# Kernel tuning notes

Hardware: AMD Instinct MI355X
Metric: run time of the kernel (lower is better)

The kernel has to match this reference:

```python
import jax, jax.numpy as jnp
import numpy as np

VOCAB = 32000
EMB_DIM = 64
BATCH, SEQ = 2, 4096


def setup_inputs() -> dict:
    key = jax.random.key(0)
    kx, kw = jax.random.split(key)
    x = jax.random.normal(kx, (BATCH, SEQ, EMB_DIM), dtype=jnp.float32)
    W = jax.random.normal(kw, (VOCAB, EMB_DIM), dtype=jnp.float32)
    return {"x": x, "W": W}


def reference(x, W):
    # x: [B, S, D] continuous embeddings; W: [V, D] embedding table.
    B, S, D = x.shape
    A = x.reshape(-1, D)                       # [N, D], N = B*S
    # cosine similarity: (A @ W^T) / (|A| |W|)
    nom = A @ W.T                              # [N, V]  (huge intermediate)
    norm_A = jnp.linalg.norm(A, axis=1)        # [N]
    norm_W = jnp.linalg.norm(W, axis=1)        # [V]
    sims = nom / (norm_A[:, None] * norm_W[None, :])
    idx = jnp.argmax(sims, axis=-1)            # [N]
    idx = idx.reshape(B, S)
    onehot = jax.nn.one_hot(idx, W.shape[0], dtype=jnp.float32)  # [B, S, V]
    return onehot
```

## Files before the change

kernel.cpp:

```cpp
#include <hip/hip_runtime.h>

#define VOCAB 32000
#define EMB 64
#define NROWS 8192
#define NSUB 500
#define SUBPAD 512
#define PAT 57
#define K2_BLOCKS 3648
#define NZ2 2048
#define K1_SETUP 125
#define K1_ZERO 875
#define K1_ITERS 28
#define K1_F4 (K1_ZERO * 256 * K1_ITERS)
#define TOTAL_F4 (NROWS * (VOCAB / 4))
#define K2_F4 (TOTAL_F4 - K1_F4)

typedef __attribute__((ext_vector_type(8))) short bf16x8;
typedef __attribute__((ext_vector_type(4))) float f32x4;
typedef float f4nt __attribute__((ext_vector_type(4)));

__device__ __forceinline__ unsigned enc_f32(float f) {
    unsigned u = __float_as_uint(f);
    return (u & 0x80000000u) ? ~u : (u | 0x80000000u);
}
__device__ __forceinline__ float dec_f32(unsigned e) {
    unsigned u = (e & 0x80000000u) ? (e & 0x7fffffffu) : ~e;
    return __uint_as_float(u);
}
__device__ __forceinline__ unsigned short f2bf(float f) {
    unsigned u = __float_as_uint(f);
    return (unsigned short)((u + 0x7fffu + ((u >> 16) & 1u)) >> 16);
}

__global__ __launch_bounds__(256) void k1_kernel(
    const float* __restrict__ x, const float* __restrict__ W,
    unsigned short* __restrict__ A16, unsigned short* __restrict__ WB16,
    float* __restrict__ invn, float* __restrict__ normA,
    float4* __restrict__ out4)
{
    const int bx = blockIdx.x;
    if (bx >= K1_SETUP) {
        const int zid = bx - K1_SETUP;
        const f4nt z = {0.f, 0.f, 0.f, 0.f};
        float4* p = out4 + (size_t)zid * 256 + threadIdx.x;
        #pragma unroll 4
        for (int j = 0; j < K1_ITERS; ++j)
            __builtin_nontemporal_store(z, (f4nt*)(p + (size_t)j * (K1_ZERO * 256)));
        return;
    }
    int i = bx * 256 + threadIdx.x;
    if (i < VOCAB) {
        const float4* w4 = (const float4*)(W + (size_t)i * EMB);
        float4 buf[16];
        float s = 0.f;
        #pragma unroll
        for (int q = 0; q < 16; ++q) {
            float4 w = w4[q]; buf[q] = w;
            s += w.x * w.x + w.y * w.y + w.z * w.z + w.w * w.w;
        }
        float inv = 1.0f / sqrtf(s);
        invn[i] = inv;
        ushort4* dst = (ushort4*)(WB16 + (size_t)i * EMB);
        #pragma unroll
        for (int q = 0; q < 16; ++q) {
            float4 w = buf[q];
            ushort4 u;
            u.x = f2bf(w.x * inv); u.y = f2bf(w.y * inv);
            u.z = f2bf(w.z * inv); u.w = f2bf(w.w * inv);
            dst[q] = u;
        }
    }
    if (i < NROWS) {
        const float4* a4 = (const float4*)(x + (size_t)i * EMB);
        float4 buf[16];
        float s = 0.f;
        #pragma unroll
        for (int q = 0; q < 16; ++q) {
            float4 a = a4[q]; buf[q] = a;
            s += a.x * a.x + a.y * a.y + a.z * a.z + a.w * a.w;
        }
        normA[i] = sqrtf(s);
        ushort4* dst = (ushort4*)(A16 + (size_t)i * EMB);
        #pragma unroll
        for (int q = 0; q < 16; ++q) {
            float4 a = buf[q];
            ushort4 u;
            u.x = f2bf(a.x); u.y = f2bf(a.y); u.z = f2bf(a.z); u.w = f2bf(a.w);
            dst[q] = u;
        }
    }
}

#define LOAD_GROUP(buf, base)                                            \
    {                                                                    \
        _Pragma("unroll")                                                \
        for (int tt = 0; tt < 4; ++tt) {                                 \
            buf[tt][0] = *(const bf16x8*)((base) + tt * 16 * EMB);       \
            buf[tt][1] = *(const bf16x8*)((base) + tt * 16 * EMB + 32);  \
        }                                                                \
    }
#define COMPUTE_GROUP(buf)                                               \
    {                                                                    \
        _Pragma("unroll")                                                \
        for (int tt = 0; tt < 4; ++tt) {                                 \
            _Pragma("unroll")                                            \
            for (int r = 0; r < 4; ++r) {                                \
                f32x4 acc = {0.f, 0.f, 0.f, 0.f};                        \
                acc = __builtin_amdgcn_mfma_f32_16x16x32_bf16(           \
                    a[r][0], buf[tt][0], acc, 0, 0, 0);                  \
                acc = __builtin_amdgcn_mfma_f32_16x16x32_bf16(           \
                    a[r][1], buf[tt][1], acc, 0, 0, 0);                  \
                _Pragma("unroll")                                        \
                for (int j = 0; j < 4; ++j)                              \
                    best[r][j] = fmaxf(best[r][j], acc[j]);              \
            }                                                            \
        }                                                                \
    }
#define STORE_SUB(sub)                                                   \
    {                                                                    \
        _Pragma("unroll")                                                \
        for (int r = 0; r < 4; ++r) {                                    \
            _Pragma("unroll")                                            \
            for (int j = 0; j < 4; ++j) {                                \
                float v = best[r][j];                                    \
                v = fmaxf(v, __shfl_xor(v, 1));                          \
                v = fmaxf(v, __shfl_xor(v, 2));                          \
                v = fmaxf(v, __shfl_xor(v, 4));                          \
                v = fmaxf(v, __shfl_xor(v, 8));                          \
                if (lr == 0)                                             \
                    pval[(size_t)(m0 + r * 16 + lg * 4 + j) * SUBPAD +   \
                         (sub)] = (unsigned short)(enc_f32(v) >> 16);    \
                best[r][j] = -3e38f;                                     \
            }                                                            \
        }                                                                \
    }

__global__ __launch_bounds__(256) void k2_kernel(
    const unsigned short* __restrict__ A16,
    const unsigned short* __restrict__ WB16,
    unsigned short* __restrict__ pval, float4* __restrict__ out4)
{
    const int bx = blockIdx.x;
    const int pat = bx / PAT, off = bx - pat * PAT;

    if (off >= 25) {
        const int zid = pat * 32 + (off - 25);
        const f4nt z = {0.f, 0.f, 0.f, 0.f};
        float4* base = out4 + K1_F4;
        unsigned i = (unsigned)zid * 256u + threadIdx.x;
        const unsigned stride = (unsigned)NZ2 * 256u;
        for (; i < (unsigned)K2_F4; i += stride)
            __builtin_nontemporal_store(z, (f4nt*)(base + i));
        return;
    }

    const int cid = pat * 25 + off;
    const int rowblk = cid & 31, chunk = cid >> 5;
    const int lane = threadIdx.x & 63, wid = threadIdx.x >> 6;
    const int lr = lane & 15, lg = lane >> 4;
    const int m0 = rowblk * 256 + wid * 64;
    const int n0 = chunk * 640;

    bf16x8 a[4][2];
    #pragma unroll
    for (int r = 0; r < 4; ++r)
        #pragma unroll
        for (int kk = 0; kk < 2; ++kk)
            a[r][kk] = *(const bf16x8*)(A16 + (size_t)(m0 + r * 16 + lr) * EMB + kk * 32 + lg * 8);

    float best[4][4];
    #pragma unroll
    for (int r = 0; r < 4; ++r)
        #pragma unroll
        for (int j = 0; j < 4; ++j) best[r][j] = -3e38f;

    const unsigned short* wb = WB16 + (size_t)(n0 + lr) * EMB + lg * 8;
    bf16x8 cb[4][2], nb[4][2];
    LOAD_GROUP(cb, wb);
    #pragma unroll
    for (int gp = 0; gp < 5; ++gp) {
        LOAD_GROUP(nb, wb + 64 * EMB);
        COMPUTE_GROUP(cb);
        STORE_SUB(chunk * 10 + gp * 2);
        wb += 64 * EMB;
        LOAD_GROUP(cb, wb + 64 * EMB);
        COMPUTE_GROUP(nb);
        STORE_SUB(chunk * 10 + gp * 2 + 1);
        wb += 64 * EMB;
    }
}

__global__ __launch_bounds__(64) void finalize_kernel(
    const float* __restrict__ x, const float* __restrict__ W,
    const float* __restrict__ invn, const unsigned short* __restrict__ pval,
    const float* __restrict__ normA, float* __restrict__ out)
{
    const int row = blockIdx.x;
    const int lane = threadIdx.x;
    __shared__ float xs[EMB];
    xs[lane] = x[(size_t)row * EMB + lane];

    const unsigned short* pr = pval + (size_t)row * SUBPAD + lane * 8;
    ushort4 v0 = *(const ushort4*)(pr);
    ushort4 v1 = *(const ushort4*)(pr + 4);
    unsigned short vals[8] = {v0.x, v0.y, v0.z, v0.w, v1.x, v1.y, v1.z, v1.w};

    unsigned mx = 0;
    #pragma unroll
    for (int k = 0; k < 8; ++k)
        if (lane * 8 + k < NSUB) mx = mx > (unsigned)vals[k] ? mx : (unsigned)vals[k];
    #pragma unroll
    for (int off = 1; off < 64; off <<= 1) {
        unsigned o = __shfl_xor(mx, off);
        mx = mx > o ? mx : o;
    }
    float thr = dec_f32(mx << 16) - 0.009f * normA[row];
    unsigned thr_enc = enc_f32(thr);

    __syncthreads();
    const float4* xs4 = (const float4*)xs;
    unsigned long long best = 0ull;

    #pragma unroll
    for (int k = 0; k < 8; ++k) {
        int sub = lane * 8 + k;
        bool c = (sub < NSUB) && ((((unsigned)vals[k] + 1u) << 16) > thr_enc);
        unsigned long long m = __ballot(c);
        while (m) {
            int src = __ffsll((long long)m) - 1;
            m &= m - 1;
            unsigned v = ((unsigned)(src * 8 + k)) * 64u + (unsigned)lane;
            const float4* w4 = (const float4*)(W + (size_t)v * EMB);
            float p0 = 0.f, p1 = 0.f, p2 = 0.f, p3 = 0.f;
            #pragma unroll
            for (int q = 0; q < 16; ++q) {
                float4 aa = xs4[q]; float4 ww = w4[q];
                p0 = fmaf(aa.x, ww.x, p0);
                p1 = fmaf(aa.y, ww.y, p1);
                p2 = fmaf(aa.z, ww.z, p2);
                p3 = fmaf(aa.w, ww.w, p3);
            }
            float s = ((p0 + p1) + (p2 + p3)) * invn[v];
            unsigned long long kk =
                ((unsigned long long)enc_f32(s) << 32) | (unsigned)(~v);
            best = best > kk ? best : kk;
        }
    }
    #pragma unroll
    for (int off = 1; off < 64; off <<= 1) {
        unsigned long long o = __shfl_xor(best, off);
        best = best > o ? best : o;
    }
    if (lane == 0)
        out[(size_t)row * VOCAB + (size_t)(unsigned)(~(unsigned)best)] = 1.0f;
}

extern "C" void kernel_launch(void* const* d_in, const int* in_sizes, int n_in,
                              void* d_out, int out_size, void* d_ws, size_t ws_size,
                              hipStream_t stream) {
    const float* x = (const float*)d_in[0];
    const float* W = (const float*)d_in[1];
    float* out = (float*)d_out;

    char* ws = (char*)d_ws;
    unsigned short* WB16 = (unsigned short*)(ws);
    unsigned short* A16  = (unsigned short*)(ws + 4096000);
    float* invn          = (float*)(ws + 5144576);
    float* normA         = (float*)(ws + 5272576);
    unsigned short* pval = (unsigned short*)(ws + 5305344);

    k1_kernel<<<dim3(K1_SETUP + K1_ZERO), dim3(256), 0, stream>>>(
        x, W, A16, WB16, invn, normA, (float4*)out);

    k2_kernel<<<dim3(K2_BLOCKS), dim3(256), 0, stream>>>(
        A16, WB16, pval, (float4*)out);

    finalize_kernel<<<dim3(NROWS), dim3(64), 0, stream>>>(
        x, W, invn, pval, normA, out);
}
```

Before: 252.5 us.

## Overlap output zeroing with finalize stage and defer one-hot writes to new kernel

Shifts part of the output zero-fill out of k1 and k2 into the finalize kernel, which now interleaves zeroing blocks with 4-row-per-block argmax refinement blocks. The winning index per row goes to a workspace buffer, and a tiny fourth kernel writes the one-hot 1.0 values after all zeroing is done. The goal is to hide memory-bound zero stores behind the latency-bound refinement work and to widen finalize blocks. The cost is an extra launch and a hardcoded K2_F4 that must agree with k2's zeroing range.

New measurement: 244.6 us. 1.03x faster.

```diff
diff --git a/kernel.cpp b/kernel.cpp
--- a/kernel.cpp
+++ b/kernel.cpp
@@ -5,15 +5,19 @@
 #define NROWS 8192
 #define NSUB 500
 #define SUBPAD 512
+#define K1_SETUP 125
+#define K1_ZERO 875
+#define K1_ITERS 21
+#define K1_F4 (K1_ZERO * 256 * K1_ITERS)
 #define PAT 57
 #define K2_BLOCKS 3648
 #define NZ2 2048
-#define K1_SETUP 125
-#define K1_ZERO 875
-#define K1_ITERS 28
-#define K1_F4 (K1_ZERO * 256 * K1_ITERS)
+#define K2_F4 51360000
+#define K3_BLOCKS 3072
+#define NZ3 1024
+#define K3_BASE (K1_F4 + K2_F4)
+#define K3_F4 9472000
 #define TOTAL_F4 (NROWS * (VOCAB / 4))
-#define K2_F4 (TOTAL_F4 - K1_F4)
 
 typedef __attribute__((ext_vector_type(8))) short bf16x8;
 typedef __attribute__((ext_vector_type(4))) float f32x4;
@@ -43,7 +47,7 @@
         const int zid = bx - K1_SETUP;
         const f4nt z = {0.f, 0.f, 0.f, 0.f};
         float4* p = out4 + (size_t)zid * 256 + threadIdx.x;
-        #pragma unroll 4
+        #pragma unroll 3
         for (int j = 0; j < K1_ITERS; ++j)
             __builtin_nontemporal_store(z, (f4nt*)(p + (size_t)j * (K1_ZERO * 256)));
         return;
@@ -190,15 +194,32 @@
     }
 }
 
-__global__ __launch_bounds__(64) void finalize_kernel(
+__global__ __launch_bounds__(256) void k3_kernel(
     const float* __restrict__ x, const float* __restrict__ W,
     const float* __restrict__ invn, const unsigned short* __restrict__ pval,
-    const float* __restrict__ normA, float* __restrict__ out)
+    const float* __restrict__ normA, unsigned long long* __restrict__ fin,
+    float4* __restrict__ out4)
 {
-    const int row = blockIdx.x;
-    const int lane = threadIdx.x;
-    __shared__ float xs[EMB];
-    xs[lane] = x[(size_t)row * EMB + lane];
+    const int bx = blockIdx.x;
+    const int pat = bx / 3, off = bx - pat * 3;
+
+    if (off == 2) {
+        const int zid = pat;
+        const f4nt z = {0.f, 0.f, 0.f, 0.f};
+        float4* base = out4 + K3_BASE;
+        unsigned i = (unsigned)zid * 256u + threadIdx.x;
+        const unsigned stride = (unsigned)NZ3 * 256u;
+        for (; i < (unsigned)K3_F4; i += stride)
+            __builtin_nontemporal_store(z, (f4nt*)(base + i));
+        return;
+    }
+
+    const int fid = pat * 2 + off;
+    const int wid = threadIdx.x >> 6, lane = threadIdx.x & 63;
+    const int row = fid * 4 + wid;
+
+    __shared__ float xs[4][EMB];
+    xs[wid][lane] = x[(size_t)row * EMB + lane];
 
     const unsigned short* pr = pval + (size_t)row * SUBPAD + lane * 8;
     ushort4 v0 = *(const ushort4*)(pr);
@@ -210,15 +231,15 @@
     for (int k = 0; k < 8; ++k)
         if (lane * 8 + k < NSUB) mx = mx > (unsigned)vals[k] ? mx : (unsigned)vals[k];
     #pragma unroll
-    for (int off = 1; off < 64; off <<= 1) {
-        unsigned o = __shfl_xor(mx, off);
+    for (int off2 = 1; off2 < 64; off2 <<= 1) {
+        unsigned o = __shfl_xor(mx, off2);
         mx = mx > o ? mx : o;
     }
     float thr = dec_f32(mx << 16) - 0.009f * normA[row];
     unsigned thr_enc = enc_f32(thr);
 
     __syncthreads();
-    const float4* xs4 = (const float4*)xs;
+    const float4* xs4 = (const float4*)xs[wid];
     unsigned long long best = 0ull;
 
     #pragma unroll
@@ -247,12 +268,18 @@
         }
     }
     #pragma unroll
-    for (int off = 1; off < 64; off <<= 1) {
-        unsigned long long o = __shfl_xor(best, off);
+    for (int off2 = 1; off2 < 64; off2 <<= 1) {
+        unsigned long long o = __shfl_xor(best, off2);
         best = best > o ? best : o;
     }
-    if (lane == 0)
-        out[(size_t)row * VOCAB + (size_t)(unsigned)(~(unsigned)best)] = 1.0f;
+    if (lane == 0) fin[row] = best;
+}
+
+__global__ void k4_kernel(const unsigned long long* __restrict__ fin,
+                          float* __restrict__ out) {
+    int row = blockIdx.x * blockDim.x + threadIdx.x;
+    if (row < NROWS)
+        out[(size_t)row * VOCAB + (size_t)(unsigned)(~(unsigned)fin[row])] = 1.0f;
 }
 
 extern "C" void kernel_launch(void* const* d_in, const int* in_sizes, int n_in,
@@ -268,6 +295,7 @@
     float* invn          = (float*)(ws + 5144576);
     float* normA         = (float*)(ws + 5272576);
     unsigned short* pval = (unsigned short*)(ws + 5305344);
+    unsigned long long* fin = (unsigned long long*)(ws + 13693952);
 
     k1_kernel<<<dim3(K1_SETUP + K1_ZERO), dim3(256), 0, stream>>>(
         x, W, A16, WB16, invn, normA, (float4*)out);
@@ -275,6 +303,8 @@
     k2_kernel<<<dim3(K2_BLOCKS), dim3(256), 0, stream>>>(
         A16, WB16, pval, (float4*)out);
 
-    finalize_kernel<<<dim3(NROWS), dim3(64), 0, stream>>>(
-        x, W, invn, pval, normA, out);
-}
+    k3_kernel<<<dim3(K3_BLOCKS), dim3(256), 0, stream>>>(
+        x, W, invn, pval, normA, fin, (float4*)out);
+
+    k4_kernel<<<dim3((NROWS + 255) / 256), dim3(256), 0, stream>>>(fin, out);
+}
```
